# Kernel tuning notes

Measured on AMD Instinct MI355X. Metric: run time of the kernel, lower is better.

Reference implementation:

```python
import jax, jax.numpy as jnp
import numpy as np

EPS = 1e-5

def group_norm(x, gamma, beta):
    # GroupNorm(num_groups=1) on [N, C]: normalize across channels per row
    mu = jnp.mean(x, axis=-1, keepdims=True)
    var = jnp.mean(jnp.square(x - mu), axis=-1, keepdims=True)
    return (x - mu) * jax.lax.rsqrt(var + EPS) * gamma + beta

def setup_inputs() -> dict:
    key = jax.random.key(0)
    ks = jax.random.split(key, 20)
    Nc, Nt, E, D = 100_000, 100_000, 500_000, 128
    f32 = jnp.float32
    s_in, s_rp, s_ctx = 1.0 / np.sqrt(D), 0.5, 1.0 / np.sqrt(2 * D)
    return {
        "context_feat": jax.random.normal(ks[0], (Nc, D), dtype=f32),
        "target_feat": jax.random.normal(ks[1], (Nt, D), dtype=f32),
        "context_pose": jax.random.normal(ks[2], (Nc, 4), dtype=f32),
        "target_pose": jax.random.normal(ks[3], (Nt, 4), dtype=f32),
        "hi": jax.random.randint(ks[4], (E,), 0, Nc, dtype=jnp.int32),
        "wi": jax.random.randint(ks[5], (E,), 0, Nt, dtype=jnp.int32),
        # params (stored [in, out]; equals torch Linear with transposed weight)
        "W_in": jax.random.normal(ks[6], (D, D), dtype=f32) * s_in,
        "W_rp": jax.random.normal(ks[7], (4, D), dtype=f32) * s_rp,
        "b_rp": jnp.zeros((D,), dtype=f32),
        "W_ctx1": jax.random.normal(ks[8], (2 * D, D), dtype=f32) * s_ctx,
        "g_ctx": jnp.ones((D,), dtype=f32),
        "be_ctx": jnp.zeros((D,), dtype=f32),
        "W_ctx2": jax.random.normal(ks[9], (D, D), dtype=f32) * s_in,
        "g_n": jnp.ones((D,), dtype=f32),
        "be_n": jnp.zeros((D,), dtype=f32),
        "W_m1": jax.random.normal(ks[10], (D, D), dtype=f32) * s_in,
        "g_m1": jnp.ones((D,), dtype=f32),
        "be_m1": jnp.zeros((D,), dtype=f32),
        "W_m2": jax.random.normal(ks[11], (D, D), dtype=f32) * s_in,
        "g_m2": jnp.ones((D,), dtype=f32),
        "be_m2": jnp.zeros((D,), dtype=f32),
    }

def reference(context_feat, target_feat, context_pose, target_pose, hi, wi,
              W_in, W_rp, b_rp, W_ctx1, g_ctx, be_ctx, W_ctx2,
              g_n, be_n, W_m1, g_m1, be_m1, W_m2, g_m2, be_m2):
    # relpose MLP on gathered pose deltas: [E,4] -> [E,128]
    dist_feat = jax.nn.relu((context_pose[hi] - target_pose[wi]) @ W_rp + b_rp)
    # ctx branch: concat gathered context feats with relpose -> [E,256] -> [E,128]
    ctx = jnp.concatenate([context_feat[hi], dist_feat], axis=-1)
    ctx = jax.nn.relu(group_norm(ctx @ W_ctx1, g_ctx, be_ctx)) @ W_ctx2
    # scatter-add onto projected target feats
    identity = target_feat
    tf = target_feat @ W_in
    tf = tf.at[wi].add(ctx)
    tf = jax.nn.relu(group_norm(tf, g_n, be_n))
    # output MLP (Linear+GN+ReLU, Linear+GN)
    tf = jax.nn.relu(group_norm(tf @ W_m1, g_m1, be_m1))
    tf = group_norm(tf @ W_m2, g_m2, be_m2)
    return jax.nn.relu(tf + identity)
```

## Files before the change

### kernel.cpp

```cpp
#include <hip/hip_runtime.h>

typedef __bf16 bf16_t;
typedef bf16_t bf16x4 __attribute__((ext_vector_type(4)));
typedef bf16_t bf16x8 __attribute__((ext_vector_type(8)));
typedef float floatx4 __attribute__((ext_vector_type(4)));

#define EPSF 1e-5f
#define DEV static __device__ __forceinline__

__global__ __launch_bounds__(256) void k_prep(
    const float* __restrict__ W_in, const float* __restrict__ W_ctx1,
    const float* __restrict__ W_ctx2, const float* __restrict__ W_m1,
    const float* __restrict__ W_m2, bf16_t* __restrict__ sw)
{
    int idx = blockIdx.x * 256 + threadIdx.x;
    const float* W; int base, ks;
    if (idx < 16384)      { W = W_in;   base = 0;     ks = 2; }
    else if (idx < 49152) { W = W_ctx1; base = 16384; ks = 3; }
    else if (idx < 65536) { W = W_ctx2; base = 49152; ks = 2; }
    else if (idx < 81920) { W = W_m1;   base = 65536; ks = 2; }
    else                  { W = W_m2;   base = 81920; ks = 2; }
    int local = idx - base;
    int j = local & 7, l = (local >> 3) & 63, rest = local >> 9;
    int s = rest & ((1 << ks) - 1), t = rest >> ks;
    int k = s * 32 + (l >> 4) * 8 + j;
    int n = t * 16 + (l & 15);
    sw[idx] = (bf16_t)W[k * 128 + n];
}

DEV void gn_rows(floatx4* acc, int lane, const float* __restrict__ gamma,
                 const float* __restrict__ beta, bool do_relu)
{
    int m = lane & 15;
    float s1[4] = {0.f,0.f,0.f,0.f}, s2[4] = {0.f,0.f,0.f,0.f};
#pragma unroll
    for (int t = 0; t < 8; ++t)
#pragma unroll
        for (int rr = 0; rr < 4; ++rr) { float v = acc[t][rr]; s1[rr] += v; s2[rr] += v*v; }
#pragma unroll
    for (int mask = 1; mask <= 8; mask <<= 1)
#pragma unroll
        for (int rr = 0; rr < 4; ++rr) {
            s1[rr] += __shfl_xor(s1[rr], mask);
            s2[rr] += __shfl_xor(s2[rr], mask);
        }
    float mean[4], inv[4];
#pragma unroll
    for (int rr = 0; rr < 4; ++rr) {
        mean[rr] = s1[rr] * (1.f/128.f);
        float var = s2[rr] * (1.f/128.f) - mean[rr]*mean[rr];
        inv[rr] = rsqrtf(var + EPSF);
    }
#pragma unroll
    for (int t = 0; t < 8; ++t) {
        int n = t*16 + m;
        float ga = gamma[n], be = beta[n];
#pragma unroll
        for (int rr = 0; rr < 4; ++rr) {
            float v = (acc[t][rr] - mean[rr]) * inv[rr] * ga + be;
            acc[t][rr] = do_relu ? fmaxf(v, 0.f) : v;
        }
    }
}

__global__ __launch_bounds__(256) void k_count(const int* __restrict__ idxs,
                                               int* __restrict__ cnt, int E)
{
    int e = blockIdx.x * 256 + threadIdx.x;
    if (e < E) atomicAdd(&cnt[idxs[e]], 1);
}

__global__ __launch_bounds__(1024) void k_scan(const int* __restrict__ cnt,
                                               int* __restrict__ off, int N)
{
    __shared__ int wsum[16];
    __shared__ int s_carry;
    int tid = threadIdx.x, lane = tid & 63, wid = tid >> 6;
    if (tid == 0) s_carry = 0;
    __syncthreads();
    for (int bs = 0; bs < N; bs += 4096) {
        int i0 = bs + tid * 4;
        int v0 = 0, v1 = 0, v2 = 0, v3 = 0;
        if (i0 + 3 < N) {
            int4 v = *(const int4*)(cnt + i0);
            v0 = v.x; v1 = v.y; v2 = v.z; v3 = v.w;
        } else {
            if (i0     < N) v0 = cnt[i0];
            if (i0 + 1 < N) v1 = cnt[i0+1];
            if (i0 + 2 < N) v2 = cnt[i0+2];
            if (i0 + 3 < N) v3 = cnt[i0+3];
        }
        int tot = v0 + v1 + v2 + v3;
        int x = tot;
#pragma unroll
        for (int d = 1; d < 64; d <<= 1) {
            int y = __shfl_up(x, d);
            if (lane >= d) x += y;
        }
        if (lane == 63) wsum[wid] = x;
        __syncthreads();
        if (wid == 0) {
            int wv = (lane < 16) ? wsum[lane] : 0;
#pragma unroll
            for (int d = 1; d < 16; d <<= 1) {
                int y = __shfl_up(wv, d);
                if (lane >= d) wv += y;
            }
            if (lane < 16) wsum[lane] = wv;
        }
        __syncthreads();
        int ebase = s_carry + ((wid > 0) ? wsum[wid-1] : 0) + (x - tot);
        if (i0 + 3 < N) {
            *(int4*)(off + i0) = make_int4(ebase, ebase+v0, ebase+v0+v1, ebase+v0+v1+v2);
        } else {
            if (i0     < N) off[i0]   = ebase;
            if (i0 + 1 < N) off[i0+1] = ebase + v0;
            if (i0 + 2 < N) off[i0+2] = ebase + v0 + v1;
            if (i0 + 3 < N) off[i0+3] = ebase + v0 + v1 + v2;
        }
        __syncthreads();
        if (tid == 0) s_carry += wsum[15];
        __syncthreads();
    }
    if (tid == 0) off[N] = s_carry;
}

__global__ __launch_bounds__(256) void k_scatter(const int* __restrict__ hi,
                                                 const int* __restrict__ off_h,
                                                 int* __restrict__ cur_h,
                                                 int* __restrict__ eidx, int E)
{
    int e = blockIdx.x * 256 + threadIdx.x;
    if (e < E) {
        int h = hi[e];
        int p = off_h[h] + atomicAdd(&cur_h[h], 1);
        eidx[p] = e;
    }
}

__global__ __launch_bounds__(256) void k_edge7(
    const float* __restrict__ cfeat, const float* __restrict__ cpose,
    const float* __restrict__ tpose, const int* __restrict__ hi,
    const int* __restrict__ wi, const int* __restrict__ eidx,
    const float* __restrict__ W_rp,
    const float* __restrict__ b_rp, const float* __restrict__ g_ctx,
    const float* __restrict__ be_ctx, const bf16_t* __restrict__ swC1,
    const int* __restrict__ off, int* __restrict__ cur,
    bf16_t* __restrict__ hbuf, int E)
{
    __shared__ alignas(16) bf16_t sH[4][2176];
    int tid = threadIdx.x, lane = tid & 63, wave = tid >> 6;
    int tb = (blockIdx.x * 4 + wave) * 16;
    int r = lane & 15, g = lane >> 4;
    int pos = min(tb + r, E - 1);
    int e = eidx[pos];
    int ci = hi[e], ti = wi[e];

    int r2 = lane >> 2, c2 = lane & 3;
    bool ev2 = (tb + r2) < E;
    int ti2 = __shfl(ti, r2);
    int dst = 0;
    if (ev2 && c2 == 0) dst = off[ti2] + atomicAdd(&cur[ti2], 1);
    dst = __shfl(dst, lane & ~3);

    floatx4 acc[8];
#pragma unroll
    for (int t = 0; t < 8; ++t) acc[t] = (floatx4){0.f,0.f,0.f,0.f};

    const float4* cf = (const float4*)(cfeat + (size_t)ci * 128);
    float4 p[8];
#pragma unroll
    for (int s = 0; s < 4; ++s) {
        p[2*s]   = cf[s*8 + g*2];
        p[2*s+1] = cf[s*8 + g*2 + 1];
    }

    float4 cp = ((const float4*)cpose)[ci];
    float4 tp = ((const float4*)tpose)[ti];
    float d0 = cp.x - tp.x, d1 = cp.y - tp.y, d2 = cp.z - tp.z, d3 = cp.w - tp.w;
#pragma unroll
    for (int sp = 0; sp < 4; ++sp) {
        int k0 = sp * 32 + g * 8;
        const float4* w0 = (const float4*)(W_rp + k0);
        const float4* w1 = (const float4*)(W_rp + 128 + k0);
        const float4* w2 = (const float4*)(W_rp + 256 + k0);
        const float4* w3 = (const float4*)(W_rp + 384 + k0);
        const float4* bb = (const float4*)(b_rp + k0);
        float o0,o1,o2,o3,o4,o5,o6,o7;
        {
            float4 a0=w0[0], a1=w1[0], a2=w2[0], a3=w3[0], ab=bb[0];
            o0 = fmaxf(d0*a0.x + d1*a1.x + d2*a2.x + d3*a3.x + ab.x, 0.f);
            o1 = fmaxf(d0*a0.y + d1*a1.y + d2*a2.y + d3*a3.y + ab.y, 0.f);
            o2 = fmaxf(d0*a0.z + d1*a1.z + d2*a2.z + d3*a3.z + ab.z, 0.f);
            o3 = fmaxf(d0*a0.w + d1*a1.w + d2*a2.w + d3*a3.w + ab.w, 0.f);
        }
        {
            float4 a0=w0[1], a1=w1[1], a2=w2[1], a3=w3[1], ab=bb[1];
            o4 = fmaxf(d0*a0.x + d1*a1.x + d2*a2.x + d3*a3.x + ab.x, 0.f);
            o5 = fmaxf(d0*a0.y + d1*a1.y + d2*a2.y + d3*a3.y + ab.y, 0.f);
            o6 = fmaxf(d0*a0.z + d1*a1.z + d2*a2.z + d3*a3.z + ab.z, 0.f);
            o7 = fmaxf(d0*a0.w + d1*a1.w + d2*a2.w + d3*a3.w + ab.w, 0.f);
        }
        bf16x8 aF = { (bf16_t)o0, (bf16_t)o1, (bf16_t)o2, (bf16_t)o3,
                      (bf16_t)o4, (bf16_t)o5, (bf16_t)o6, (bf16_t)o7 };
        int s = 4 + sp;
#pragma unroll
        for (int t = 0; t < 8; ++t) {
            bf16x8 bF = *(const bf16x8*)&swC1[(size_t)((t*8 + s)*64 + lane)*8];
            acc[t] = __builtin_amdgcn_mfma_f32_16x16x32_bf16(aF, bF, acc[t], 0, 0, 0);
        }
    }
#pragma unroll
    for (int s = 0; s < 4; ++s) {
        float4 v0 = p[2*s], v1 = p[2*s+1];
        bf16x8 aF = { (bf16_t)v0.x, (bf16_t)v0.y, (bf16_t)v0.z, (bf16_t)v0.w,
                      (bf16_t)v1.x, (bf16_t)v1.y, (bf16_t)v1.z, (bf16_t)v1.w };
#pragma unroll
        for (int t = 0; t < 8; ++t) {
            bf16x8 bF = *(const bf16x8*)&swC1[(size_t)((t*8 + s)*64 + lane)*8];
            acc[t] = __builtin_amdgcn_mfma_f32_16x16x32_bf16(aF, bF, acc[t], 0, 0, 0);
        }
    }
    gn_rows(acc, lane, g_ctx, be_ctx, true);

#pragma unroll
    for (int t = 0; t < 8; ++t)
#pragma unroll
        for (int rr = 0; rr < 4; ++rr)
            sH[wave][(g*4 + rr)*136 + t*16 + r] = (bf16_t)acc[t][rr];

    if (ev2) {
        bf16_t* hp = hbuf + (size_t)dst * 128 + c2 * 32;
#pragma unroll
        for (int i = 0; i < 4; ++i)
            *(bf16x8*)(hp + i*8) = *(const bf16x8*)&sH[wave][r2*136 + c2*32 + i*8];
    }
}

__global__ __launch_bounds__(256) void k_out3(
    const float* __restrict__ tfeat, const bf16_t* __restrict__ hbuf,
    const int* __restrict__ off,
    const float* __restrict__ g_n, const float* __restrict__ be_n,
    const float* __restrict__ g_m1, const float* __restrict__ be_m1,
    const float* __restrict__ g_m2, const float* __restrict__ be_m2,
    const bf16_t* __restrict__ swIn, const bf16_t* __restrict__ swC2,
    const bf16_t* __restrict__ swM1, const bf16_t* __restrict__ swM2,
    float* __restrict__ out, int Nt)
{
    __shared__ alignas(16) bf16_t sB[4][2176];
    int tid = threadIdx.x, lane = tid & 63, wave = tid >> 6;
    int tb = (blockIdx.x*4 + wave)*16;
    int r = lane & 15, g = lane >> 4;
    int grow = tb + r;
    bool rv = grow < Nt;
    int rclamp = rv ? grow : (Nt - 1);

    const float4* cf = (const float4*)(tfeat + (size_t)rclamp * 128);
    float4 p[8];
#pragma unroll
    for (int s = 0; s < 4; ++s) {
        p[2*s]   = cf[s*8 + g*2];
        p[2*s+1] = cf[s*8 + g*2 + 1];
    }

    float sums[32];
#pragma unroll
    for (int i = 0; i < 32; ++i) sums[i] = 0.f;
    int jb = rv ? off[grow] : 0, je = rv ? off[grow+1] : 0;
    for (int jr = jb; jr < je; ++jr) {
        const bf16_t* hp = hbuf + (size_t)jr*128 + g*8;
#pragma unroll
        for (int s = 0; s < 4; ++s) {
            bf16x8 hv = *(const bf16x8*)(hp + s*32);
#pragma unroll
            for (int q = 0; q < 8; ++q) sums[s*8+q] += (float)hv[q];
        }
    }
#pragma unroll
    for (int s = 0; s < 4; ++s) {
        bf16x8 ah = { (bf16_t)sums[s*8+0], (bf16_t)sums[s*8+1],
                      (bf16_t)sums[s*8+2], (bf16_t)sums[s*8+3],
                      (bf16_t)sums[s*8+4], (bf16_t)sums[s*8+5],
                      (bf16_t)sums[s*8+6], (bf16_t)sums[s*8+7] };
        *(bf16x8*)&sB[wave][r*136 + s*32 + g*8] = ah;
    }

    floatx4 acc[8];
#pragma unroll
    for (int t = 0; t < 8; ++t) acc[t] = (floatx4){0.f,0.f,0.f,0.f};
#pragma unroll
    for (int s = 0; s < 4; ++s) {
        bf16x8 aH = *(const bf16x8*)&sB[wave][r*136 + s*32 + g*8];
#pragma unroll
        for (int t = 0; t < 8; ++t) {
            bf16x8 bF = *(const bf16x8*)&swC2[((t*4+s)*64 + lane)*8];
            acc[t] = __builtin_amdgcn_mfma_f32_16x16x32_bf16(aH, bF, acc[t], 0, 0, 0);
        }
        float4 v0 = p[2*s], v1 = p[2*s+1];
        bf16x8 aF = { (bf16_t)v0.x, (bf16_t)v0.y, (bf16_t)v0.z, (bf16_t)v0.w,
                      (bf16_t)v1.x, (bf16_t)v1.y, (bf16_t)v1.z, (bf16_t)v1.w };
#pragma unroll
        for (int t = 0; t < 8; ++t) {
            bf16x8 bF = *(const bf16x8*)&swIn[((t*4+s)*64 + lane)*8];
            acc[t] = __builtin_amdgcn_mfma_f32_16x16x32_bf16(aF, bF, acc[t], 0, 0, 0);
        }
    }
    gn_rows(acc, lane, g_n, be_n, true);

#pragma unroll
    for (int t = 0; t < 8; ++t)
#pragma unroll
        for (int rr = 0; rr < 4; ++rr)
            sB[wave][(g*4 + rr)*136 + t*16 + r] = (bf16_t)acc[t][rr];
#pragma unroll
    for (int t = 0; t < 8; ++t) acc[t] = (floatx4){0.f,0.f,0.f,0.f};
#pragma unroll
    for (int s = 0; s < 4; ++s) {
        bf16x8 aF = *(const bf16x8*)&sB[wave][r*136 + s*32 + g*8];
#pragma unroll
        for (int t = 0; t < 8; ++t) {
            bf16x8 bF = *(const bf16x8*)&swM1[((t*4+s)*64 + lane)*8];
            acc[t] = __builtin_amdgcn_mfma_f32_16x16x32_bf16(aF, bF, acc[t], 0, 0, 0);
        }
    }
    gn_rows(acc, lane, g_m1, be_m1, true);

#pragma unroll
    for (int t = 0; t < 8; ++t)
#pragma unroll
        for (int rr = 0; rr < 4; ++rr)
            sB[wave][(g*4 + rr)*136 + t*16 + r] = (bf16_t)acc[t][rr];
#pragma unroll
    for (int t = 0; t < 8; ++t) acc[t] = (floatx4){0.f,0.f,0.f,0.f};
#pragma unroll
    for (int s = 0; s < 4; ++s) {
        bf16x8 aF = *(const bf16x8*)&sB[wave][r*136 + s*32 + g*8];
#pragma unroll
        for (int t = 0; t < 8; ++t) {
            bf16x8 bF = *(const bf16x8*)&swM2[((t*4+s)*64 + lane)*8];
            acc[t] = __builtin_amdgcn_mfma_f32_16x16x32_bf16(aF, bF, acc[t], 0, 0, 0);
        }
    }
    gn_rows(acc, lane, g_m2, be_m2, false);

#pragma unroll
    for (int t = 0; t < 8; ++t) {
        int n = t*16 + r;
#pragma unroll
        for (int rr = 0; rr < 4; ++rr) {
            int row = tb + g*4 + rr;
            if (row < Nt) {
                float v = acc[t][rr] + tfeat[(size_t)row*128 + n];
                out[(size_t)row*128 + n] = fmaxf(v, 0.f);
            }
        }
    }
}

__global__ __launch_bounds__(256) void k_gemm_in(
    const float* __restrict__ tfeat, const bf16_t* __restrict__ swW,
    float* __restrict__ tf, int Nt)
{
    __shared__ alignas(16) bf16_t sA[4][2048];
    int tid = threadIdx.x, lane = tid & 63, wave = tid >> 6;

    int tb = (blockIdx.x * 4 + wave) * 16;
    int r = lane >> 2, cb = (lane & 3) * 32;
    int grow = tb + r;
    bool rv = grow < Nt;
    const float4* src = (const float4*)(tfeat + (size_t)(rv ? grow : 0) * 128 + cb);
#pragma unroll
    for (int i = 0; i < 8; ++i) {
        float4 v = rv ? src[i] : make_float4(0.f,0.f,0.f,0.f);
        int k = cb + 4*i;
        int s = k >> 5, q = (k >> 3) & 3, j = k & 7;
        bf16x4 pk = { (bf16_t)v.x, (bf16_t)v.y, (bf16_t)v.z, (bf16_t)v.w };
        *(bf16x4*)&sA[wave][(s*64 + q*16 + r)*8 + j] = pk;
    }
    __syncthreads();
    int m = lane & 15, g = lane >> 4;
    bf16x8 aF[4];
#pragma unroll
    for (int s = 0; s < 4; ++s) aF[s] = *(const bf16x8*)&sA[wave][(s*64 + lane)*8];
#pragma unroll
    for (int t = 0; t < 8; ++t) {
        floatx4 a = {0.f,0.f,0.f,0.f};
#pragma unroll
        for (int s = 0; s < 4; ++s) {
            bf16x8 bF = *(const bf16x8*)&swW[((t*4+s)*64 + lane)*8];
            a = __builtin_amdgcn_mfma_f32_16x16x32_bf16(aF[s], bF, a, 0, 0, 0);
        }
#pragma unroll
        for (int rr = 0; rr < 4; ++rr) {
            int row = tb + g*4 + rr;
            if (row < Nt) tf[(size_t)row*128 + t*16 + m] = a[rr];
        }
    }
}

__global__ __launch_bounds__(256) void k_edge_old(
    const float* __restrict__ cfeat, const float* __restrict__ cpose,
    const float* __restrict__ tpose, const int* __restrict__ hi,
    const int* __restrict__ wi, const float* __restrict__ W_rp,
    const float* __restrict__ b_rp, const float* __restrict__ g_ctx,
    const float* __restrict__ be_ctx, const bf16_t* __restrict__ swC1,
    const bf16_t* __restrict__ swC2, float* __restrict__ tf, int E)
{
    __shared__ alignas(16) bf16_t sA[4][4096];
    int tid = threadIdx.x, lane = tid & 63, wave = tid >> 6;

    int tb = (blockIdx.x * 4 + wave) * 16;
    int r = lane >> 2, cb = (lane & 3) * 32;
    int e = min(tb + r, E - 1);
    int ci = hi[e], ti = wi[e];
    const float4* src = (const float4*)(cfeat + (size_t)ci * 128 + cb);
#pragma unroll
    for (int i = 0; i < 8; ++i) {
        float4 v = src[i];
        int k = cb + 4*i;
        int s = k >> 5, q = (k >> 3) & 3, j = k & 7;
        bf16x4 pk = { (bf16_t)v.x, (bf16_t)v.y, (bf16_t)v.z, (bf16_t)v.w };
        *(bf16x4*)&sA[wave][(s*64 + q*16 + r)*8 + j] = pk;
    }
    float4 cp = ((const float4*)cpose)[ci];
    float4 tp = ((const float4*)tpose)[ti];
    float d0 = cp.x - tp.x, d1 = cp.y - tp.y, d2 = cp.z - tp.z, d3 = cp.w - tp.w;
#pragma unroll
    for (int i = 0; i < 8; ++i) {
        int cc = cb + 4*i;
        float4 w0 = *(const float4*)(W_rp + cc);
        float4 w1 = *(const float4*)(W_rp + 128 + cc);
        float4 w2 = *(const float4*)(W_rp + 256 + cc);
        float4 w3 = *(const float4*)(W_rp + 384 + cc);
        float4 bb = *(const float4*)(b_rp + cc);
        float o0 = fmaxf(d0*w0.x + d1*w1.x + d2*w2.x + d3*w3.x + bb.x, 0.f);
        float o1 = fmaxf(d0*w0.y + d1*w1.y + d2*w2.y + d3*w3.y + bb.y, 0.f);
        float o2 = fmaxf(d0*w0.z + d1*w1.z + d2*w2.z + d3*w3.z + bb.z, 0.f);
        float o3 = fmaxf(d0*w0.w + d1*w1.w + d2*w2.w + d3*w3.w + bb.w, 0.f);
        int k = 128 + cc;
        int s = k >> 5, q = (k >> 3) & 3, j = k & 7;
        bf16x4 pk = { (bf16_t)o0, (bf16_t)o1, (bf16_t)o2, (bf16_t)o3 };
        *(bf16x4*)&sA[wave][(s*64 + q*16 + r)*8 + j] = pk;
    }
    __syncthreads();

    int m = lane & 15, g = lane >> 4;
    bf16x8 aF[8];
#pragma unroll
    for (int s = 0; s < 8; ++s) aF[s] = *(const bf16x8*)&sA[wave][(s*64 + lane)*8];
    floatx4 acc[8];
#pragma unroll
    for (int t = 0; t < 8; ++t) {
        floatx4 a = {0.f,0.f,0.f,0.f};
#pragma unroll
        for (int s = 0; s < 8; ++s) {
            bf16x8 bF = *(const bf16x8*)&swC1[(size_t)((t*8+s)*64 + lane)*8];
            a = __builtin_amdgcn_mfma_f32_16x16x32_bf16(aF[s], bF, a, 0, 0, 0);
        }
        acc[t] = a;
    }
    gn_rows(acc, lane, g_ctx, be_ctx, true);
    __syncthreads();
#pragma unroll
    for (int t = 0; t < 8; ++t) {
        int n = t*16 + m;
        int s = n >> 5, q = (n >> 3) & 3, j = n & 7;
#pragma unroll
        for (int rr = 0; rr < 4; ++rr)
            sA[wave][(s*64 + q*16 + (g*4+rr))*8 + j] = (bf16_t)acc[t][rr];
    }
    __syncthreads();
    bf16x8 aF2[4];
#pragma unroll
    for (int s = 0; s < 4; ++s) aF2[s] = *(const bf16x8*)&sA[wave][(s*64 + lane)*8];
    int dstrow[4]; bool vald[4];
#pragma unroll
    for (int rr = 0; rr < 4; ++rr) {
        int ee = tb + g*4 + rr;
        vald[rr] = ee < E;
        dstrow[rr] = vald[rr] ? wi[ee] : 0;
    }
#pragma unroll
    for (int t = 0; t < 8; ++t) {
        floatx4 a = {0.f,0.f,0.f,0.f};
#pragma unroll
        for (int s = 0; s < 4; ++s) {
            bf16x8 bF = *(const bf16x8*)&swC2[((t*4+s)*64 + lane)*8];
            a = __builtin_amdgcn_mfma_f32_16x16x32_bf16(aF2[s], bF, a, 0, 0, 0);
        }
#pragma unroll
        for (int rr = 0; rr < 4; ++rr) {
            if (vald[rr])
                atomicAdd(&tf[(size_t)dstrow[rr]*128 + t*16 + m], a[rr]);
        }
    }
}

__global__ __launch_bounds__(256) void k_out_old(
    const float* __restrict__ tf, const float* __restrict__ identity,
    const float* __restrict__ g_n, const float* __restrict__ be_n,
    const float* __restrict__ g_m1, const float* __restrict__ be_m1,
    const float* __restrict__ g_m2, const float* __restrict__ be_m2,
    const bf16_t* __restrict__ swM1, const bf16_t* __restrict__ swM2,
    float* __restrict__ out, int Nt)
{
    __shared__ alignas(16) bf16_t sA[4][2048];
    int tid = threadIdx.x, lane = tid & 63, wave = tid >> 6;

    int tb = (blockIdx.x*4 + wave)*16;
    int r = lane >> 2, cb = (lane & 3)*32;
    int grow = tb + r;
    bool rv = grow < Nt;
    const float4* src = (const float4*)(tf + (size_t)(rv ? grow : 0)*128 + cb);
    float vals[32];
    float ls = 0.f, lq = 0.f;
#pragma unroll
    for (int i = 0; i < 8; ++i) {
        float4 v = rv ? src[i] : make_float4(0.f,0.f,0.f,0.f);
        vals[4*i+0]=v.x; vals[4*i+1]=v.y; vals[4*i+2]=v.z; vals[4*i+3]=v.w;
        ls += v.x+v.y+v.z+v.w;
        lq += v.x*v.x+v.y*v.y+v.z*v.z+v.w*v.w;
    }
    ls += __shfl_xor(ls,1); lq += __shfl_xor(lq,1);
    ls += __shfl_xor(ls,2); lq += __shfl_xor(lq,2);
    float mean = ls*(1.f/128.f);
    float inv = rsqrtf(lq*(1.f/128.f) - mean*mean + EPSF);
#pragma unroll
    for (int i = 0; i < 8; ++i) {
        int cc = cb + 4*i;
        float4 ga = *(const float4*)(g_n + cc);
        float4 be = *(const float4*)(be_n + cc);
        float o0 = fmaxf((vals[4*i+0]-mean)*inv*ga.x + be.x, 0.f);
        float o1 = fmaxf((vals[4*i+1]-mean)*inv*ga.y + be.y, 0.f);
        float o2 = fmaxf((vals[4*i+2]-mean)*inv*ga.z + be.z, 0.f);
        float o3 = fmaxf((vals[4*i+3]-mean)*inv*ga.w + be.w, 0.f);
        int s = cc >> 5, q = (cc >> 3) & 3, j = cc & 7;
        bf16x4 pk = { (bf16_t)o0, (bf16_t)o1, (bf16_t)o2, (bf16_t)o3 };
        *(bf16x4*)&sA[wave][(s*64 + q*16 + r)*8 + j] = pk;
    }
    __syncthreads();
    int m = lane & 15, g = lane >> 4;
    bf16x8 aF[4];
#pragma unroll
    for (int s = 0; s < 4; ++s) aF[s] = *(const bf16x8*)&sA[wave][(s*64 + lane)*8];
    floatx4 acc[8];
#pragma unroll
    for (int t = 0; t < 8; ++t) {
        floatx4 a = {0.f,0.f,0.f,0.f};
#pragma unroll
        for (int s = 0; s < 4; ++s) {
            bf16x8 bF = *(const bf16x8*)&swM1[((t*4+s)*64 + lane)*8];
            a = __builtin_amdgcn_mfma_f32_16x16x32_bf16(aF[s], bF, a, 0, 0, 0);
        }
        acc[t] = a;
    }
    gn_rows(acc, lane, g_m1, be_m1, true);
    __syncthreads();
#pragma unroll
    for (int t = 0; t < 8; ++t) {
        int n = t*16 + m;
        int s = n >> 5, q = (n >> 3) & 3, j = n & 7;
#pragma unroll
        for (int rr = 0; rr < 4; ++rr)
            sA[wave][(s*64 + q*16 + (g*4+rr))*8 + j] = (bf16_t)acc[t][rr];
    }
    __syncthreads();
#pragma unroll
    for (int s = 0; s < 4; ++s) aF[s] = *(const bf16x8*)&sA[wave][(s*64 + lane)*8];
#pragma unroll
    for (int t = 0; t < 8; ++t) {
        floatx4 a = {0.f,0.f,0.f,0.f};
#pragma unroll
        for (int s = 0; s < 4; ++s) {
            bf16x8 bF = *(const bf16x8*)&swM2[((t*4+s)*64 + lane)*8];
            a = __builtin_amdgcn_mfma_f32_16x16x32_bf16(aF[s], bF, a, 0, 0, 0);
        }
        acc[t] = a;
    }
    gn_rows(acc, lane, g_m2, be_m2, false);
#pragma unroll
    for (int t = 0; t < 8; ++t) {
        int n = t*16 + m;
#pragma unroll
        for (int rr = 0; rr < 4; ++rr) {
            int row = tb + g*4 + rr;
            if (row < Nt) {
                float v = acc[t][rr] + identity[(size_t)row*128 + n];
                out[(size_t)row*128 + n] = fmaxf(v, 0.f);
            }
        }
    }
}

extern "C" void kernel_launch(void* const* d_in, const int* in_sizes, int n_in,
                              void* d_out, int out_size, void* d_ws, size_t ws_size,
                              hipStream_t stream)
{
    const float* cfeat  = (const float*)d_in[0];
    const float* tfeat  = (const float*)d_in[1];
    const float* cpose  = (const float*)d_in[2];
    const float* tpose  = (const float*)d_in[3];
    const int*   hi     = (const int*)d_in[4];
    const int*   wi     = (const int*)d_in[5];
    const float* W_in   = (const float*)d_in[6];
    const float* W_rp   = (const float*)d_in[7];
    const float* b_rp   = (const float*)d_in[8];
    const float* W_ctx1 = (const float*)d_in[9];
    const float* g_ctx  = (const float*)d_in[10];
    const float* be_ctx = (const float*)d_in[11];
    const float* W_ctx2 = (const float*)d_in[12];
    const float* g_n    = (const float*)d_in[13];
    const float* be_n   = (const float*)d_in[14];
    const float* W_m1   = (const float*)d_in[15];
    const float* g_m1   = (const float*)d_in[16];
    const float* be_m1  = (const float*)d_in[17];
    const float* W_m2   = (const float*)d_in[18];
    const float* g_m2   = (const float*)d_in[19];
    const float* be_m2  = (const float*)d_in[20];

    int Nt = in_sizes[1] / 128;
    int Nc = in_sizes[0] / 128;
    int E  = in_sizes[4];
    float* outp = (float*)d_out;

    char* base = (char*)d_ws;
    size_t o = 98304 * sizeof(bf16_t);
    o = (o + 255) & ~(size_t)255;
    size_t o_cnt = o; o += (size_t)Nt * 4;
    o = (o + 255) & ~(size_t)255;
    size_t o_off = o; o += ((size_t)Nt + 1) * 4;
    o = (o + 255) & ~(size_t)255;
    size_t o_cur = o; o += (size_t)Nt * 4;
    o = (o + 255) & ~(size_t)255;
    size_t o_cnth = o; o += (size_t)Nc * 4;
    o = (o + 255) & ~(size_t)255;
    size_t o_offh = o; o += ((size_t)Nc + 1) * 4;
    o = (o + 255) & ~(size_t)255;
    size_t o_curh = o; o += (size_t)Nc * 4;
    o = (o + 255) & ~(size_t)255;
    size_t o_eidx = o; o += (size_t)E * 4;
    o = (o + 255) & ~(size_t)255;
    size_t o_h = o; o += (size_t)E * 128 * sizeof(bf16_t);

    if (ws_size >= o) {
        bf16_t* sw    = (bf16_t*)base;
        int*    cnt   = (int*)(base + o_cnt);
        int*    off   = (int*)(base + o_off);
        int*    cur   = (int*)(base + o_cur);
        int*    cnth  = (int*)(base + o_cnth);
        int*    offh  = (int*)(base + o_offh);
        int*    curh  = (int*)(base + o_curh);
        int*    eidx  = (int*)(base + o_eidx);
        bf16_t* hbuf  = (bf16_t*)(base + o_h);
        bf16_t* swIn = sw;
        bf16_t* swC1 = sw + 16384;
        bf16_t* swC2 = sw + 49152;
        bf16_t* swM1 = sw + 65536;
        bf16_t* swM2 = sw + 81920;

        hipMemsetAsync(cnt, 0, (size_t)Nt * 4, stream);
        hipMemsetAsync(cur, 0, (size_t)Nt * 4, stream);
        hipMemsetAsync(cnth, 0, (size_t)Nc * 4, stream);
        hipMemsetAsync(curh, 0, (size_t)Nc * 4, stream);
        k_prep<<<384, 256, 0, stream>>>(W_in, W_ctx1, W_ctx2, W_m1, W_m2, sw);
        k_count<<<(E + 255) / 256, 256, 0, stream>>>(wi, cnt, E);
        k_scan<<<1, 1024, 0, stream>>>(cnt, off, Nt);
        k_count<<<(E + 255) / 256, 256, 0, stream>>>(hi, cnth, E);
        k_scan<<<1, 1024, 0, stream>>>(cnth, offh, Nc);
        k_scatter<<<(E + 255) / 256, 256, 0, stream>>>(hi, offh, curh, eidx, E);
        k_edge7<<<(E + 63) / 64, 256, 0, stream>>>(cfeat, cpose, tpose, hi, wi,
                                                   eidx, W_rp, b_rp, g_ctx, be_ctx,
                                                   swC1, off, cur, hbuf, E);
        k_out3<<<(Nt + 63) / 64, 256, 0, stream>>>(tfeat, hbuf, off,
                                                   g_n, be_n, g_m1, be_m1,
                                                   g_m2, be_m2,
                                                   swIn, swC2, swM1, swM2,
                                                   outp, Nt);
    } else {
        float*  tf = (float*)d_ws;
        bf16_t* sw = (bf16_t*)((char*)d_ws + (size_t)Nt * 128 * sizeof(float));
        bf16_t* swIn = sw;
        bf16_t* swC1 = sw + 16384;
        bf16_t* swC2 = sw + 49152;
        bf16_t* swM1 = sw + 65536;
        bf16_t* swM2 = sw + 81920;

        k_prep<<<384, 256, 0, stream>>>(W_in, W_ctx1, W_ctx2, W_m1, W_m2, sw);
        k_gemm_in<<<(Nt + 63) / 64, 256, 0, stream>>>(tfeat, swIn, tf, Nt);
        k_edge_old<<<(E + 63) / 64, 256, 0, stream>>>(cfeat, cpose, tpose, hi, wi,
                                                      W_rp, b_rp, g_ctx, be_ctx,
                                                      swC1, swC2, tf, E);
        k_out_old<<<(Nt + 63) / 64, 256, 0, stream>>>(tf, tfeat, g_n, be_n,
                                                      g_m1, be_m1, g_m2, be_m2,
                                                      swM1, swM2, outp, Nt);
    }
}
```

Baseline: 557.0 us.

## Drop hi-sorted edge ordering and parallelize the offset scan across blocks

Removes the second counting-sort pass that ordered edges by context index (count, scan, scatter over hi), so the edge kernel now processes edges in original order. The single-block serial prefix scan over target counts becomes a three-kernel multi-block scan. Slot assignment by target now happens in a separate pass that writes per-edge destinations, replacing the atomics inside the edge kernel. The cost is less locality on context-feature gathers, since edges are no longer grouped by context row.

Result: faster. 474.0 us (-14.9%).

```diff
diff --git a/kernel.cpp b/kernel.cpp
--- a/kernel.cpp
+++ b/kernel.cpp
@@ -70,98 +70,122 @@
     if (e < E) atomicAdd(&cnt[idxs[e]], 1);
 }
 
-__global__ __launch_bounds__(1024) void k_scan(const int* __restrict__ cnt,
-                                               int* __restrict__ off, int N)
+__global__ __launch_bounds__(1024) void k_scanA(const int* __restrict__ cnt,
+                                                int* __restrict__ off,
+                                                int* __restrict__ bsum, int N)
 {
     __shared__ int wsum[16];
-    __shared__ int s_carry;
     int tid = threadIdx.x, lane = tid & 63, wid = tid >> 6;
-    if (tid == 0) s_carry = 0;
-    __syncthreads();
-    for (int bs = 0; bs < N; bs += 4096) {
-        int i0 = bs + tid * 4;
-        int v0 = 0, v1 = 0, v2 = 0, v3 = 0;
-        if (i0 + 3 < N) {
-            int4 v = *(const int4*)(cnt + i0);
-            v0 = v.x; v1 = v.y; v2 = v.z; v3 = v.w;
-        } else {
-            if (i0     < N) v0 = cnt[i0];
-            if (i0 + 1 < N) v1 = cnt[i0+1];
-            if (i0 + 2 < N) v2 = cnt[i0+2];
-            if (i0 + 3 < N) v3 = cnt[i0+3];
-        }
-        int tot = v0 + v1 + v2 + v3;
-        int x = tot;
-#pragma unroll
-        for (int d = 1; d < 64; d <<= 1) {
-            int y = __shfl_up(x, d);
-            if (lane >= d) x += y;
-        }
-        if (lane == 63) wsum[wid] = x;
-        __syncthreads();
-        if (wid == 0) {
-            int wv = (lane < 16) ? wsum[lane] : 0;
-#pragma unroll
-            for (int d = 1; d < 16; d <<= 1) {
-                int y = __shfl_up(wv, d);
-                if (lane >= d) wv += y;
-            }
-            if (lane < 16) wsum[lane] = wv;
-        }
-        __syncthreads();
-        int ebase = s_carry + ((wid > 0) ? wsum[wid-1] : 0) + (x - tot);
-        if (i0 + 3 < N) {
-            *(int4*)(off + i0) = make_int4(ebase, ebase+v0, ebase+v0+v1, ebase+v0+v1+v2);
-        } else {
-            if (i0     < N) off[i0]   = ebase;
-            if (i0 + 1 < N) off[i0+1] = ebase + v0;
-            if (i0 + 2 < N) off[i0+2] = ebase + v0 + v1;
-            if (i0 + 3 < N) off[i0+3] = ebase + v0 + v1 + v2;
-        }
-        __syncthreads();
-        if (tid == 0) s_carry += wsum[15];
-        __syncthreads();
-    }
-    if (tid == 0) off[N] = s_carry;
-}
-
-__global__ __launch_bounds__(256) void k_scatter(const int* __restrict__ hi,
-                                                 const int* __restrict__ off_h,
-                                                 int* __restrict__ cur_h,
-                                                 int* __restrict__ eidx, int E)
+    int i0 = blockIdx.x * 4096 + tid * 4;
+    int v0 = 0, v1 = 0, v2 = 0, v3 = 0;
+    if (i0 + 3 < N) {
+        int4 v = *(const int4*)(cnt + i0);
+        v0 = v.x; v1 = v.y; v2 = v.z; v3 = v.w;
+    } else {
+        if (i0     < N) v0 = cnt[i0];
+        if (i0 + 1 < N) v1 = cnt[i0+1];
+        if (i0 + 2 < N) v2 = cnt[i0+2];
+        if (i0 + 3 < N) v3 = cnt[i0+3];
+    }
+    int tot = v0 + v1 + v2 + v3;
+    int x = tot;
+#pragma unroll
+    for (int d = 1; d < 64; d <<= 1) {
+        int y = __shfl_up(x, d);
+        if (lane >= d) x += y;
+    }
+    if (lane == 63) wsum[wid] = x;
+    __syncthreads();
+    if (wid == 0) {
+        int wv = (lane < 16) ? wsum[lane] : 0;
+#pragma unroll
+        for (int d = 1; d < 16; d <<= 1) {
+            int y = __shfl_up(wv, d);
+            if (lane >= d) wv += y;
+        }
+        if (lane < 16) wsum[lane] = wv;
+    }
+    __syncthreads();
+    int ebase = ((wid > 0) ? wsum[wid-1] : 0) + (x - tot);
+    if (i0 + 3 < N) {
+        *(int4*)(off + i0) = make_int4(ebase, ebase+v0, ebase+v0+v1, ebase+v0+v1+v2);
+    } else {
+        if (i0     < N) off[i0]   = ebase;
+        if (i0 + 1 < N) off[i0+1] = ebase + v0;
+        if (i0 + 2 < N) off[i0+2] = ebase + v0 + v1;
+        if (i0 + 3 < N) off[i0+3] = ebase + v0 + v1 + v2;
+    }
+    if (tid == 0) bsum[blockIdx.x] = wsum[15];
+}
+
+__global__ __launch_bounds__(1024) void k_scanB(int* __restrict__ bsum,
+                                                int* __restrict__ off,
+                                                int NB, int N)
+{
+    __shared__ int wsum[16];
+    int tid = threadIdx.x, lane = tid & 63, wid = tid >> 6;
+    int v = (tid < NB) ? bsum[tid] : 0;
+    int x = v;
+#pragma unroll
+    for (int d = 1; d < 64; d <<= 1) {
+        int y = __shfl_up(x, d);
+        if (lane >= d) x += y;
+    }
+    if (lane == 63) wsum[wid] = x;
+    __syncthreads();
+    if (wid == 0) {
+        int wv = (lane < 16) ? wsum[lane] : 0;
+#pragma unroll
+        for (int d = 1; d < 16; d <<= 1) {
+            int y = __shfl_up(wv, d);
+            if (lane >= d) wv += y;
+        }
+        if (lane < 16) wsum[lane] = wv;
+    }
+    __syncthreads();
+    int excl = ((wid > 0) ? wsum[wid-1] : 0) + (x - v);
+    if (tid < NB) bsum[tid] = excl;
+    if (tid == 0) off[N] = wsum[15];
+}
+
+__global__ __launch_bounds__(256) void k_scanC(int* __restrict__ off,
+                                               const int* __restrict__ bsum, int N)
+{
+    int i = blockIdx.x * 256 + threadIdx.x;
+    if (i < N) off[i] += bsum[i >> 12];
+}
+
+__global__ __launch_bounds__(256) void k_slots(const int* __restrict__ wi,
+                                               const int* __restrict__ off,
+                                               int* __restrict__ cur,
+                                               int* __restrict__ dst, int E)
 {
     int e = blockIdx.x * 256 + threadIdx.x;
     if (e < E) {
-        int h = hi[e];
-        int p = off_h[h] + atomicAdd(&cur_h[h], 1);
-        eidx[p] = e;
-    }
-}
-
-__global__ __launch_bounds__(256) void k_edge7(
+        int w = wi[e];
+        dst[e] = off[w] + atomicAdd(&cur[w], 1);
+    }
+}
+
+__global__ __launch_bounds__(256) void k_edge8(
     const float* __restrict__ cfeat, const float* __restrict__ cpose,
     const float* __restrict__ tpose, const int* __restrict__ hi,
-    const int* __restrict__ wi, const int* __restrict__ eidx,
+    const int* __restrict__ wi, const int* __restrict__ dst,
     const float* __restrict__ W_rp,
     const float* __restrict__ b_rp, const float* __restrict__ g_ctx,
     const float* __restrict__ be_ctx, const bf16_t* __restrict__ swC1,
-    const int* __restrict__ off, int* __restrict__ cur,
     bf16_t* __restrict__ hbuf, int E)
 {
     __shared__ alignas(16) bf16_t sH[4][2176];
     int tid = threadIdx.x, lane = tid & 63, wave = tid >> 6;
     int tb = (blockIdx.x * 4 + wave) * 16;
     int r = lane & 15, g = lane >> 4;
-    int pos = min(tb + r, E - 1);
-    int e = eidx[pos];
+    int e = min(tb + r, E - 1);
     int ci = hi[e], ti = wi[e];
 
     int r2 = lane >> 2, c2 = lane & 3;
     bool ev2 = (tb + r2) < E;
-    int ti2 = __shfl(ti, r2);
-    int dst = 0;
-    if (ev2 && c2 == 0) dst = off[ti2] + atomicAdd(&cur[ti2], 1);
-    dst = __shfl(dst, lane & ~3);
+    int dstv = dst[min(tb + r2, E - 1)];
 
     floatx4 acc[8];
 #pragma unroll
@@ -230,7 +254,7 @@
             sH[wave][(g*4 + rr)*136 + t*16 + r] = (bf16_t)acc[t][rr];
 
     if (ev2) {
-        bf16_t* hp = hbuf + (size_t)dst * 128 + c2 * 32;
+        bf16_t* hp = hbuf + (size_t)dstv * 128 + c2 * 32;
 #pragma unroll
         for (int i = 0; i < 4; ++i)
             *(bf16x8*)(hp + i*8) = *(const bf16x8*)&sH[wave][r2*136 + c2*32 + i*8];
@@ -619,7 +643,6 @@
     const float* be_m2  = (const float*)d_in[20];
 
     int Nt = in_sizes[1] / 128;
-    int Nc = in_sizes[0] / 128;
     int E  = in_sizes[4];
     float* outp = (float*)d_out;
 
@@ -632,25 +655,21 @@
     o = (o + 255) & ~(size_t)255;
     size_t o_cur = o; o += (size_t)Nt * 4;
     o = (o + 255) & ~(size_t)255;
-    size_t o_cnth = o; o += (size_t)Nc * 4;
+    size_t o_bsum = o; o += 1024 * 4;
     o = (o + 255) & ~(size_t)255;
-    size_t o_offh = o; o += ((size_t)Nc + 1) * 4;
-    o = (o + 255) & ~(size_t)255;
-    size_t o_curh = o; o += (size_t)Nc * 4;
-    o = (o + 255) & ~(size_t)255;
-    size_t o_eidx = o; o += (size_t)E * 4;
+    size_t o_dst = o; o += (size_t)E * 4;
     o = (o + 255) & ~(size_t)255;
     size_t o_h = o; o += (size_t)E * 128 * sizeof(bf16_t);
 
-    if (ws_size >= o) {
+    int NB = (Nt + 4095) / 4096;
+
+    if (ws_size >= o && NB <= 1024) {
         bf16_t* sw    = (bf16_t*)base;
         int*    cnt   = (int*)(base + o_cnt);
         int*    off   = (int*)(base + o_off);
         int*    cur   = (int*)(base + o_cur);
-        int*    cnth  = (int*)(base + o_cnth);
-        int*    offh  = (int*)(base + o_offh);
-        int*    curh  = (int*)(base + o_curh);
-        int*    eidx  = (int*)(base + o_eidx);
+        int*    bsum  = (int*)(base + o_bsum);
+        int*    dst   = (int*)(base + o_dst);
         bf16_t* hbuf  = (bf16_t*)(base + o_h);
         bf16_t* swIn = sw;
         bf16_t* swC1 = sw + 16384;
@@ -660,17 +679,15 @@
 
         hipMemsetAsync(cnt, 0, (size_t)Nt * 4, stream);
         hipMemsetAsync(cur, 0, (size_t)Nt * 4, stream);
-        hipMemsetAsync(cnth, 0, (size_t)Nc * 4, stream);
-        hipMemsetAsync(curh, 0, (size_t)Nc * 4, stream);
         k_prep<<<384, 256, 0, stream>>>(W_in, W_ctx1, W_ctx2, W_m1, W_m2, sw);
         k_count<<<(E + 255) / 256, 256, 0, stream>>>(wi, cnt, E);
-        k_scan<<<1, 1024, 0, stream>>>(cnt, off, Nt);
-        k_count<<<(E + 255) / 256, 256, 0, stream>>>(hi, cnth, E);
-        k_scan<<<1, 1024, 0, stream>>>(cnth, offh, Nc);
-        k_scatter<<<(E + 255) / 256, 256, 0, stream>>>(hi, offh, curh, eidx, E);
-        k_edge7<<<(E + 63) / 64, 256, 0, stream>>>(cfeat, cpose, tpose, hi, wi,
-                                                   eidx, W_rp, b_rp, g_ctx, be_ctx,
-                                                   swC1, off, cur, hbuf, E);
+        k_scanA<<<NB, 1024, 0, stream>>>(cnt, off, bsum, Nt);
+        k_scanB<<<1, 1024, 0, stream>>>(bsum, off, NB, Nt);
+        k_scanC<<<(Nt + 255) / 256, 256, 0, stream>>>(off, bsum, Nt);
+        k_slots<<<(E + 255) / 256, 256, 0, stream>>>(wi, off, cur, dst, E);
+        k_edge8<<<(E + 63) / 64, 256, 0, stream>>>(cfeat, cpose, tpose, hi, wi,
+                                                   dst, W_rp, b_rp, g_ctx, be_ctx,
+                                                   swC1, hbuf, E);
         k_out3<<<(Nt + 63) / 64, 256, 0, stream>>>(tfeat, hbuf, off,
                                                    g_n, be_n, g_m1, be_m1,
                                                    g_m2, be_m2,
```
